# Optimization experiments

Hardware: AMD Instinct MI355X
Metric: run time of the kernel (lower is better)

The kernel has to match this reference:

```python
import jax, jax.numpy as jnp
import numpy as np

EPS = 1e-5


def setup_inputs() -> dict:
    key = jax.random.key(0)
    ks = jax.random.split(key, 6)
    B, H, W, C = 4, 64, 64, 64
    x_in = jax.random.normal(ks[0], (B, H, W, C), dtype=jnp.float32)
    scale = 1.0 / np.sqrt(C)
    w1 = jax.random.normal(ks[1], (C, C), dtype=jnp.float32) * scale
    w2 = jax.random.normal(ks[2], (C, C), dtype=jnp.float32) * scale
    w3 = jax.random.normal(ks[3], (C, C), dtype=jnp.float32) * scale
    w4 = jax.random.normal(ks[4], (C, C), dtype=jnp.float32) * scale
    zeros = jnp.zeros((C,), dtype=jnp.float32)
    return {
        "x_in": x_in,
        "w1": w1, "w2": w2, "w3": w3, "w4": w4,
        "b1": zeros, "b2": zeros, "b3": zeros, "b4": zeros,
        "gamma": jnp.ones((C,), dtype=jnp.float32),
        "beta": zeros,
    }


def reference(x_in, w1, w2, w3, w4, b1, b2, b3, b4, gamma, beta):
    B, H, W, C = x_in.shape
    # BatchNorm over batch + spatial dims, per channel (training-mode batch stats)
    mean = jnp.mean(x_in, axis=(0, 1, 2))            # [C]
    var = jnp.var(x_in, axis=(0, 1, 2))              # [C]
    x = (x_in - mean) * jax.lax.rsqrt(var + EPS) * gamma + beta
    # QKV projections
    q = jnp.einsum('bhwc,cC->bhwC', x, w1) + b1
    k = jnp.einsum('bhwc,cC->bhwC', x, w2) + b2
    v = jnp.einsum('bhwc,cC->bhwC', x, w3) + b3
    # Full spatial attention: [B, H, W, H, W]
    sdpa = jnp.einsum('bhwc,bHWc->bhwHW', q, k) / jnp.sqrt(jnp.float32(C))
    sdpa = jax.nn.softmax(sdpa.reshape(B, H, W, H * W), axis=-1)
    sdpa = sdpa.reshape(B, H, W, H, W)
    x = jnp.einsum('bhwHW,bHWc->bhwc', sdpa, v)
    # Output projection + residual
    x = jnp.einsum('bhwc,cC->bhwC', x, w4) + b4
    return x + x_in
```

## Files before the change

### kernel.cpp

```cpp
#include <hip/hip_runtime.h>

typedef _Float16 f16;
typedef _Float16 half8 __attribute__((ext_vector_type(8)));
typedef float f32x4 __attribute__((ext_vector_type(4)));
typedef float f32x16 __attribute__((ext_vector_type(16)));
typedef unsigned u32x4 __attribute__((ext_vector_type(4)));

#define LDW 72

__global__ __launch_bounds__(256) void k_bnstats(const float* __restrict__ x, float* __restrict__ part){
    __shared__ float red[512];
    int t = threadIdx.x;
    int c = t & 63, rg = t >> 6;
    int rb = blockIdx.x * 64;
    float s = 0.f, s2 = 0.f;
    for(int r = rg; r < 64; r += 4){
        float v = x[(rb + r) * 64 + c];
        s += v; s2 += v * v;
    }
    red[t] = s; red[256 + t] = s2;
    __syncthreads();
    if(t < 128){
        int c2 = t & 63, h = t >> 6;
        float a = red[h * 256 + c2] + red[h * 256 + c2 + 64] + red[h * 256 + c2 + 128] + red[h * 256 + c2 + 192];
        part[blockIdx.x * 128 + t] = a;
    }
}

__global__ __launch_bounds__(256) void k_qkv(
    const float* __restrict__ x,
    const float* __restrict__ w1, const float* __restrict__ w2, const float* __restrict__ w3,
    const float* __restrict__ b1, const float* __restrict__ b2, const float* __restrict__ b3,
    const float* __restrict__ gamma, const float* __restrict__ beta,
    const float* __restrict__ part,
    f16* __restrict__ Q, f16* __restrict__ Kx, f16* __restrict__ Vt){
    __shared__ f16 wT[3 * 64 * LDW];
    __shared__ float sc[64], sh[64], bb[3][64];
    __shared__ float psum[128];
    int t = threadIdx.x;
    for(int i = t; i < 3 * 4096; i += 256){
        int j = i >> 12, e = i & 4095, k = e >> 6, n = e & 63;
        const float* wp = (j == 0) ? w1 : ((j == 1) ? w2 : w3);
        wT[j * 64 * LDW + n * LDW + k] = (f16)wp[e];
    }
    if(t < 128){
        float a0 = 0.f, a1 = 0.f, a2 = 0.f, a3 = 0.f;
        for(int b = 0; b < 256; b += 4){
            a0 += part[b * 128 + t];       a1 += part[(b + 1) * 128 + t];
            a2 += part[(b + 2) * 128 + t]; a3 += part[(b + 3) * 128 + t];
        }
        psum[t] = (a0 + a1) + (a2 + a3);
    }
    __syncthreads();
    if(t < 64){
        float mean = psum[t] * (1.f / 16384.f);
        float var  = psum[64 + t] * (1.f / 16384.f) - mean * mean;
        float s = gamma[t] * rsqrtf(var + 1e-5f);
        sc[t] = s;
        sh[t] = beta[t] - mean * s;
        bb[0][t] = b1[t]; bb[1][t] = b2[t]; bb[2][t] = b3[t];
    }
    __syncthreads();
    int w = t >> 6, lane = t & 63, quad = lane >> 4, l15 = lane & 15;
    int rowb = blockIdx.x * 64 + w * 16;
    int arow = rowb + l15;
    half8 a[2];
    #pragma unroll
    for(int kc = 0; kc < 2; kc++){
        f32x4 x0 = *(const f32x4*)&x[arow * 64 + kc * 32 + quad * 8];
        f32x4 x1 = *(const f32x4*)&x[arow * 64 + kc * 32 + quad * 8 + 4];
        half8 h;
        #pragma unroll
        for(int j = 0; j < 8; j++){
            int c = kc * 32 + quad * 8 + j;
            float xv = (j < 4) ? x0[j & 3] : x1[j & 3];
            h[j] = (f16)(xv * sc[c] + sh[c]);
        }
        a[kc] = h;
    }
    const f32x4 vzero = {0.f, 0.f, 0.f, 0.f};
    f32x4 acc[3][4];
    #pragma unroll
    for(int m = 0; m < 3; m++){
        #pragma unroll
        for(int nt = 0; nt < 4; nt++){
            acc[m][nt] = vzero;
            #pragma unroll
            for(int kc = 0; kc < 2; kc++){
                half8 bfr = *(half8*)&wT[m * 64 * LDW + (nt * 16 + l15) * LDW + kc * 32 + quad * 8];
                acc[m][nt] = __builtin_amdgcn_mfma_f32_16x16x32_f16(a[kc], bfr, acc[m][nt], 0, 0, 0);
            }
        }
    }
    const float qs = 0.18033688011112043f;
    #pragma unroll
    for(int nt = 0; nt < 4; nt++){
        #pragma unroll
        for(int r = 0; r < 4; r++){
            int row = rowb + quad * 4 + r;
            int col = nt * 16 + l15;
            Q[row * 64 + col]  = (f16)((acc[0][nt][r] + bb[0][col]) * qs);
            Kx[row * 64 + col] = (f16)(acc[1][nt][r] + bb[1][col]);
            Vt[((row >> 12) * 64 + col) * 4096 + (row & 4095)] = (f16)(acc[2][nt][r] + bb[2][col]);
        }
    }
}

__global__ __launch_bounds__(256, 4) void k_attn(
    const f16* __restrict__ Q, const f16* __restrict__ Kx, const f16* __restrict__ Vt,
    f16* __restrict__ Oph, float* __restrict__ lw){
    __shared__ f16 KV[2][2 * 64 * LDW];
    __shared__ float lred[4][32];
    int t = threadIdx.x;
    int kq = blockIdx.x & 7, qg = blockIdx.x >> 3;
    int b = qg >> 5;
    int w = t >> 6, lane = t & 63, l31 = lane & 31, hi = lane >> 5;
    int qrow0 = qg * 128 + w * 32;
    const int BUF = 2 * 64 * LDW;

    half8 aq[4];
    #pragma unroll
    for(int dc = 0; dc < 4; dc++)
        aq[dc] = *(const half8*)&Q[(qrow0 + l31) * 64 + dc * 16 + hi * 8];

    const f16* gsrc[4];
    int loff[4], gstep[4];
    #pragma unroll
    for(int i = 0; i < 4; i++){
        int idx = t + i * 256;
        int rr = (idx >> 3) & 63, c8 = idx & 7, kt0 = kq * 8;
        if(idx < 512){
            loff[i] = rr * LDW + c8 * 8;
            gsrc[i] = &Kx[(b * 4096 + kt0 * 64 + rr) * 64 + c8 * 8];
            gstep[i] = 64 * 64;
        } else {
            loff[i] = 64 * LDW + rr * LDW + c8 * 8;
            gsrc[i] = &Vt[(b * 64 + rr) * 4096 + kt0 * 64 + c8 * 8];
            gstep[i] = 64;
        }
    }
    half8 pre[4];
    #pragma unroll
    for(int i = 0; i < 4; i++){ pre[i] = *(const half8*)gsrc[i]; gsrc[i] += gstep[i]; }
    #pragma unroll
    for(int i = 0; i < 4; i++) *(half8*)&KV[0][loff[i]] = pre[i];

    f32x16 o[2];
    #pragma unroll
    for(int dt = 0; dt < 2; dt++)
        #pragma unroll
        for(int r = 0; r < 16; r++) o[dt][r] = 0.f;
    float lp = 0.f;

    __syncthreads();
    int cur = 0;
    for(int j = 0; j < 8; j++){
        if(j < 7){
            #pragma unroll
            for(int i = 0; i < 4; i++){ pre[i] = *(const half8*)gsrc[i]; gsrc[i] += gstep[i]; }
        }
        const f16* Kb = &KV[0][0] + cur * BUF;
        const f16* Vb = Kb + 64 * LDW;
        #pragma unroll
        for(int kt = 0; kt < 2; kt++){
            half8 ak[4];
            #pragma unroll
            for(int dc = 0; dc < 4; dc++)
                ak[dc] = *(const half8*)&Kb[(kt * 32 + l31) * LDW + dc * 16 + hi * 8];
            half8 vb[2][2];
            #pragma unroll
            for(int kc = 0; kc < 2; kc++)
                #pragma unroll
                for(int dt = 0; dt < 2; dt++)
                    vb[kc][dt] = *(const half8*)&Vb[(dt * 32 + l31) * LDW + kt * 32 + kc * 16 + hi * 8];
            f32x16 s;
            #pragma unroll
            for(int r = 0; r < 16; r++) s[r] = 0.f;
            #pragma unroll
            for(int dc = 0; dc < 4; dc++)
                s = __builtin_amdgcn_mfma_f32_32x32x16_f16(ak[dc], aq[dc], s, 0, 0, 0);
            float pf[16], ls = 0.f;
            #pragma unroll
            for(int r = 0; r < 16; r++){
                float p = __builtin_amdgcn_exp2f(fminf(s[r], 15.f));
                pf[r] = p; ls += p;
            }
            lp += ls;
            unsigned wv[4][2];
            #pragma unroll
            for(int g = 0; g < 4; g++){
                wv[g][0] = __builtin_bit_cast(unsigned, __builtin_amdgcn_cvt_pkrtz(pf[4*g+0], pf[4*g+1]));
                wv[g][1] = __builtin_bit_cast(unsigned, __builtin_amdgcn_cvt_pkrtz(pf[4*g+2], pf[4*g+3]));
            }
            #pragma unroll
            for(int kc = 0; kc < 2; kc++){
                unsigned x0 = wv[2*kc][0], y0 = wv[2*kc+1][0];
                unsigned x1 = wv[2*kc][1], y1 = wv[2*kc+1][1];
                asm("v_permlane32_swap_b32 %0, %1" : "+v"(x0), "+v"(y0));
                asm("v_permlane32_swap_b32 %0, %1" : "+v"(x1), "+v"(y1));
                u32x4 pw = {x0, x1, y0, y1};
                half8 pa = __builtin_bit_cast(half8, pw);
                #pragma unroll
                for(int dt = 0; dt < 2; dt++)
                    o[dt] = __builtin_amdgcn_mfma_f32_32x32x16_f16(pa, vb[kc][dt], o[dt], 0, 0, 0);
            }
        }
        if(j < 7){
            f16* wb = &KV[0][0] + (cur ^ 1) * BUF;
            #pragma unroll
            for(int i = 0; i < 4; i++) *(half8*)(wb + loff[i]) = pre[i];
        }
        cur ^= 1;
        __syncthreads();
    }
    {
        float v = lp + __shfl_xor(lp, 32);
        if(hi == 0){
            int row = qrow0 + l31;
            lw[kq * 16384 + row] = v;
            lred[w][l31] = __builtin_amdgcn_rcpf(v);
        }
    }
    #pragma unroll
    for(int r = 0; r < 16; r++){
        int qrl = (r & 3) + 8 * (r >> 2) + 4 * hi;
        float inv = lred[w][qrl];
        int row = qrow0 + qrl;
        #pragma unroll
        for(int dt = 0; dt < 2; dt++)
            Oph[kq * 1048576 + row * 64 + dt * 32 + l31] = (f16)(o[dt][r] * inv);
    }
}

__global__ __launch_bounds__(256) void k_merge(
    const f16* __restrict__ Oph, const float* __restrict__ lw,
    const float* __restrict__ w4, const float* __restrict__ b4,
    const float* __restrict__ x, float* __restrict__ out){
    __shared__ f16 Om[64 * LDW];
    __shared__ f16 wT[64 * LDW];
    __shared__ float b4f[64];
    int t = threadIdx.x;
    int rb = blockIdx.x * 64;
    for(int i = t; i < 4096; i += 256){
        int k = i >> 6, n = i & 63;
        wT[n * LDW + k] = (f16)w4[i];
    }
    if(t < 64) b4f[t] = b4[t];
    for(int i = t; i < 512; i += 256){
        int row = i >> 3, c8 = i & 7;
        int gr = rb + row;
        float num[8] = {0.f,0.f,0.f,0.f,0.f,0.f,0.f,0.f};
        float den = 0.f;
        #pragma unroll
        for(int s = 0; s < 8; s++){
            float li = lw[s * 16384 + gr];
            half8 ov = *(const half8*)&Oph[s * 1048576 + gr * 64 + c8 * 8];
            #pragma unroll
            for(int j = 0; j < 8; j++) num[j] += li * (float)ov[j];
            den += li;
        }
        float invd = 1.f / den;
        #pragma unroll
        for(int j = 0; j < 8; j++) Om[row * LDW + c8 * 8 + j] = (f16)(num[j] * invd);
    }
    __syncthreads();
    int w = t >> 6, lane = t & 63, quad = lane >> 4, l15 = lane & 15;
    half8 a[2];
    #pragma unroll
    for(int kc = 0; kc < 2; kc++)
        a[kc] = *(half8*)&Om[(w * 16 + l15) * LDW + kc * 32 + quad * 8];
    #pragma unroll
    for(int nt = 0; nt < 4; nt++){
        f32x4 y = {0.f, 0.f, 0.f, 0.f};
        #pragma unroll
        for(int kc = 0; kc < 2; kc++){
            half8 bfr = *(half8*)&wT[(nt * 16 + l15) * LDW + kc * 32 + quad * 8];
            y = __builtin_amdgcn_mfma_f32_16x16x32_f16(a[kc], bfr, y, 0, 0, 0);
        }
        #pragma unroll
        for(int r = 0; r < 4; r++){
            int row = rb + w * 16 + quad * 4 + r;
            int col = nt * 16 + l15;
            out[row * 64 + col] = y[r] + b4f[col] + x[row * 64 + col];
        }
    }
}

extern "C" void kernel_launch(void* const* d_in, const int* in_sizes, int n_in,
                              void* d_out, int out_size, void* d_ws, size_t ws_size,
                              hipStream_t stream){
    (void)in_sizes; (void)n_in; (void)out_size; (void)ws_size;
    const float* x  = (const float*)d_in[0];
    const float* w1 = (const float*)d_in[1];
    const float* w2 = (const float*)d_in[2];
    const float* w3 = (const float*)d_in[3];
    const float* w4 = (const float*)d_in[4];
    const float* b1 = (const float*)d_in[5];
    const float* b2 = (const float*)d_in[6];
    const float* b3 = (const float*)d_in[7];
    const float* b4 = (const float*)d_in[8];
    const float* gm = (const float*)d_in[9];
    const float* bt = (const float*)d_in[10];
    char* ws = (char*)d_ws;
    f16* Q    = (f16*)(ws);
    f16* Kx   = (f16*)(ws + (size_t)(2u << 20));
    f16* Vt   = (f16*)(ws + (size_t)(4u << 20));
    float* part = (float*)(ws + (size_t)(6u << 20));
    f16* Oph  = (f16*)(ws + (size_t)(8u << 20));
    float* lwp = (float*)(ws + (size_t)(24u << 20));

    hipLaunchKernelGGL(k_bnstats, dim3(256),  dim3(256), 0, stream, x, part);
    hipLaunchKernelGGL(k_qkv,     dim3(256),  dim3(256), 0, stream, x, w1, w2, w3, b1, b2, b3, gm, bt, part, Q, Kx, Vt);
    hipLaunchKernelGGL(k_attn,    dim3(1024), dim3(256), 0, stream, Q, Kx, Vt, Oph, lwp);
    hipLaunchKernelGGL(k_merge,   dim3(256),  dim3(256), 0, stream, Oph, lwp, w4, b4, x, (float*)d_out);
}
```

Before: 130.9 us.

## Load K/V fragments directly from global into registers, dropping LDS staging

The attention kernel stops staging K and V tiles through double-buffered shared memory with block-wide barriers. Each wave now loads its own K fragments from global memory straight into registers, double-buffered one step ahead, and loads V fragments in the same iteration that uses them. The 16-step loop is fully unrolled and the occupancy hint drops from 4 to 3 blocks to allow more registers. This removes LDS writes and reads and all per-tile __syncthreads, but each of the four waves now fetches the same K/V data, roughly quadrupling L2/global traffic, and V load latency is less hidden.

```diff
diff --git a/kernel.cpp b/kernel.cpp
--- a/kernel.cpp
+++ b/kernel.cpp
@@ -106,44 +106,31 @@
     }
 }
 
-__global__ __launch_bounds__(256, 4) void k_attn(
+__global__ __launch_bounds__(256, 3) void k_attn(
     const f16* __restrict__ Q, const f16* __restrict__ Kx, const f16* __restrict__ Vt,
     f16* __restrict__ Oph, float* __restrict__ lw){
-    __shared__ f16 KV[2][2 * 64 * LDW];
     __shared__ float lred[4][32];
     int t = threadIdx.x;
     int kq = blockIdx.x & 7, qg = blockIdx.x >> 3;
     int b = qg >> 5;
     int w = t >> 6, lane = t & 63, l31 = lane & 31, hi = lane >> 5;
     int qrow0 = qg * 128 + w * 32;
-    const int BUF = 2 * 64 * LDW;
+    int kv0 = kq * 512;
 
     half8 aq[4];
     #pragma unroll
     for(int dc = 0; dc < 4; dc++)
         aq[dc] = *(const half8*)&Q[(qrow0 + l31) * 64 + dc * 16 + hi * 8];
 
-    const f16* gsrc[4];
-    int loff[4], gstep[4];
-    #pragma unroll
-    for(int i = 0; i < 4; i++){
-        int idx = t + i * 256;
-        int rr = (idx >> 3) & 63, c8 = idx & 7, kt0 = kq * 8;
-        if(idx < 512){
-            loff[i] = rr * LDW + c8 * 8;
-            gsrc[i] = &Kx[(b * 4096 + kt0 * 64 + rr) * 64 + c8 * 8];
-            gstep[i] = 64 * 64;
-        } else {
-            loff[i] = 64 * LDW + rr * LDW + c8 * 8;
-            gsrc[i] = &Vt[(b * 64 + rr) * 4096 + kt0 * 64 + c8 * 8];
-            gstep[i] = 64;
-        }
-    }
-    half8 pre[4];
-    #pragma unroll
-    for(int i = 0; i < 4; i++){ pre[i] = *(const half8*)gsrc[i]; gsrc[i] += gstep[i]; }
-    #pragma unroll
-    for(int i = 0; i < 4; i++) *(half8*)&KV[0][loff[i]] = pre[i];
+    const f16* kp  = Kx + (size_t)(b * 4096 + kv0 + l31) * 64 + hi * 8;
+    const f16* vp0 = Vt + (size_t)(b * 64 + l31) * 4096 + kv0 + hi * 8;
+    const f16* vp1 = Vt + (size_t)(b * 64 + 32 + l31) * 4096 + kv0 + hi * 8;
+
+    half8 kf[2][4];
+    half8 vf[2][2];
+    #pragma unroll
+    for(int dc = 0; dc < 4; dc++) kf[0][dc] = *(const half8*)(kp + dc * 16);
+    kp += 32 * 64;
 
     f32x16 o[2];
     #pragma unroll
@@ -152,66 +139,51 @@
         for(int r = 0; r < 16; r++) o[dt][r] = 0.f;
     float lp = 0.f;
 
-    __syncthreads();
-    int cur = 0;
-    for(int j = 0; j < 8; j++){
-        if(j < 7){
-            #pragma unroll
-            for(int i = 0; i < 4; i++){ pre[i] = *(const half8*)gsrc[i]; gsrc[i] += gstep[i]; }
-        }
-        const f16* Kb = &KV[0][0] + cur * BUF;
-        const f16* Vb = Kb + 64 * LDW;
-        #pragma unroll
-        for(int kt = 0; kt < 2; kt++){
-            half8 ak[4];
-            #pragma unroll
-            for(int dc = 0; dc < 4; dc++)
-                ak[dc] = *(const half8*)&Kb[(kt * 32 + l31) * LDW + dc * 16 + hi * 8];
-            half8 vb[2][2];
-            #pragma unroll
-            for(int kc = 0; kc < 2; kc++)
-                #pragma unroll
-                for(int dt = 0; dt < 2; dt++)
-                    vb[kc][dt] = *(const half8*)&Vb[(dt * 32 + l31) * LDW + kt * 32 + kc * 16 + hi * 8];
-            f32x16 s;
-            #pragma unroll
-            for(int r = 0; r < 16; r++) s[r] = 0.f;
-            #pragma unroll
-            for(int dc = 0; dc < 4; dc++)
-                s = __builtin_amdgcn_mfma_f32_32x32x16_f16(ak[dc], aq[dc], s, 0, 0, 0);
-            float pf[16], ls = 0.f;
-            #pragma unroll
-            for(int r = 0; r < 16; r++){
-                float p = __builtin_amdgcn_exp2f(fminf(s[r], 15.f));
-                pf[r] = p; ls += p;
-            }
-            lp += ls;
-            unsigned wv[4][2];
-            #pragma unroll
-            for(int g = 0; g < 4; g++){
-                wv[g][0] = __builtin_bit_cast(unsigned, __builtin_amdgcn_cvt_pkrtz(pf[4*g+0], pf[4*g+1]));
-                wv[g][1] = __builtin_bit_cast(unsigned, __builtin_amdgcn_cvt_pkrtz(pf[4*g+2], pf[4*g+3]));
-            }
-            #pragma unroll
-            for(int kc = 0; kc < 2; kc++){
-                unsigned x0 = wv[2*kc][0], y0 = wv[2*kc+1][0];
-                unsigned x1 = wv[2*kc][1], y1 = wv[2*kc+1][1];
-                asm("v_permlane32_swap_b32 %0, %1" : "+v"(x0), "+v"(y0));
-                asm("v_permlane32_swap_b32 %0, %1" : "+v"(x1), "+v"(y1));
-                u32x4 pw = {x0, x1, y0, y1};
-                half8 pa = __builtin_bit_cast(half8, pw);
-                #pragma unroll
-                for(int dt = 0; dt < 2; dt++)
-                    o[dt] = __builtin_amdgcn_mfma_f32_32x32x16_f16(pa, vb[kc][dt], o[dt], 0, 0, 0);
-            }
-        }
-        if(j < 7){
-            f16* wb = &KV[0][0] + (cur ^ 1) * BUF;
-            #pragma unroll
-            for(int i = 0; i < 4; i++) *(half8*)(wb + loff[i]) = pre[i];
-        }
-        cur ^= 1;
-        __syncthreads();
+    #pragma unroll
+    for(int j = 0; j < 16; j++){
+        const int cur = j & 1;
+        #pragma unroll
+        for(int kc = 0; kc < 2; kc++){
+            vf[kc][0] = *(const half8*)(vp0 + kc * 16);
+            vf[kc][1] = *(const half8*)(vp1 + kc * 16);
+        }
+        vp0 += 32; vp1 += 32;
+        if(j < 15){
+            #pragma unroll
+            for(int dc = 0; dc < 4; dc++) kf[cur ^ 1][dc] = *(const half8*)(kp + dc * 16);
+            kp += 32 * 64;
+        }
+        f32x16 s;
+        #pragma unroll
+        for(int r = 0; r < 16; r++) s[r] = 0.f;
+        #pragma unroll
+        for(int dc = 0; dc < 4; dc++)
+            s = __builtin_amdgcn_mfma_f32_32x32x16_f16(kf[cur][dc], aq[dc], s, 0, 0, 0);
+        float pf[16], ls = 0.f;
+        #pragma unroll
+        for(int r = 0; r < 16; r++){
+            float p = __builtin_amdgcn_exp2f(fminf(s[r], 15.f));
+            pf[r] = p; ls += p;
+        }
+        lp += ls;
+        unsigned wv[4][2];
+        #pragma unroll
+        for(int g = 0; g < 4; g++){
+            wv[g][0] = __builtin_bit_cast(unsigned, __builtin_amdgcn_cvt_pkrtz(pf[4*g+0], pf[4*g+1]));
+            wv[g][1] = __builtin_bit_cast(unsigned, __builtin_amdgcn_cvt_pkrtz(pf[4*g+2], pf[4*g+3]));
+        }
+        #pragma unroll
+        for(int kc = 0; kc < 2; kc++){
+            unsigned x0 = wv[2*kc][0], y0 = wv[2*kc+1][0];
+            unsigned x1 = wv[2*kc][1], y1 = wv[2*kc+1][1];
+            asm("v_permlane32_swap_b32 %0, %1" : "+v"(x0), "+v"(y0));
+            asm("v_permlane32_swap_b32 %0, %1" : "+v"(x1), "+v"(y1));
+            u32x4 pw = {x0, x1, y0, y1};
+            half8 pa = __builtin_bit_cast(half8, pw);
+            #pragma unroll
+            for(int dt = 0; dt < 2; dt++)
+                o[dt] = __builtin_amdgcn_mfma_f32_32x32x16_f16(pa, vf[kc][dt], o[dt], 0, 0, 0);
+        }
     }
     {
         float v = lp + __shfl_xor(lp, 32);
@@ -221,6 +193,7 @@
             lred[w][l31] = __builtin_amdgcn_rcpf(v);
         }
     }
+    __builtin_amdgcn_s_waitcnt(0);
     #pragma unroll
     for(int r = 0; r < 16; r++){
         int qrl = (r & 3) + 8 * (r >> 2) + 4 * hi;
```

New measurement: 165.7 us. +26.6%, slower.
